# Kernel tuning notes

Hardware: AMD Instinct MI355X
Metric: run time of the kernel (lower is better)

## Reference

```python
import jax, jax.numpy as jnp
import numpy as np

B, S, E = 32, 128, 128
NQ, NS = 100000, 512
QN, SN = 4, 10
S_MAX = 4
NEG = -1e30


def setup_inputs() -> dict:
    key = jax.random.key(0)
    ks = jax.random.split(key, 24)
    def nrm(k, shape, sc):
        return jax.random.normal(k, shape, jnp.float32) * sc
    inp = {}
    inp['question'] = jax.random.randint(ks[0], (B, S), 0, NQ, jnp.int32)
    inp['response'] = jax.random.randint(ks[1], (B, S), 0, 2, jnp.int32)
    inp['mask'] = jax.random.randint(ks[2], (B, S), 0, 2, jnp.int32)
    inp['q_neighbors'] = jax.random.randint(ks[3], (NQ, QN), 0, NS, jnp.int32)
    inp['s_neighbors'] = jax.random.randint(ks[4], (NS, SN), 0, NQ, jnp.int32)
    sidx = jax.random.randint(ks[5], (NQ, S_MAX), 0, NS, jnp.int32)
    inp['qs_table'] = jnp.zeros((NQ, NS), jnp.float32).at[jnp.arange(NQ)[:, None], sidx].set(1.0)
    inp['emb_q'] = nrm(ks[6], (NQ, E), 1.0)
    inp['emb_s'] = nrm(ks[7], (NS, E), 1.0)
    inp['emb_r'] = nrm(ks[8], (2, E), 1.0)
    s_in = 1.0 / np.sqrt(2 * E).astype(np.float32)
    s_e = 1.0 / np.sqrt(E).astype(np.float32)
    inp['W_ih'] = nrm(ks[9], (4 * E, 2 * E), s_in)
    inp['b_ih'] = nrm(ks[10], (4 * E,), s_in)
    inp['b_hh'] = nrm(ks[11], (4 * E,), s_in)
    inp['W_agg'] = nrm(ks[12], (3, E, E), s_e)
    inp['b_agg'] = nrm(ks[13], (3, E), s_e)
    inp['W_last'] = nrm(ks[14], (E, E), s_e)
    inp['b_last'] = nrm(ks[15], (E,), s_e)
    inp['W_query'] = nrm(ks[16], (E, E), s_e)
    inp['b_query'] = nrm(ks[17], (E,), s_e)
    inp['W_key'] = nrm(ks[18], (E, E), s_e)
    inp['b_key'] = nrm(ks[19], (E,), s_e)
    inp['w_W'] = nrm(ks[20], (2 * E,), s_in)
    inp['b_W'] = nrm(ks[21], (), s_in)
    return inp


def _forward(question, response, mask, q_neighbors, s_neighbors, qs_table,
             emb_q, emb_s, emb_r, W_ih, b_ih, b_hh, W_agg, b_agg, W_last, b_last,
             W_query, b_query, W_key, b_key, w_W, b_W):
    Bq, Sq = question.shape
    Ed = emb_q.shape[1]
    AGG = W_agg.shape[0]
    w_q, w_k = w_W[:Ed], w_W[Ed:]
    c_pad = jnp.tanh(b_query) @ w_k  # attention logit piece of an all-zero padded state
    pos = jnp.arange(Sq)

    def step(state_history, xs):
        t, q_t, r_t, m_t, q_next = xs
        # ---- multi-hop neighbor gather (q -> s -> q -> s) ----
        n1 = q_neighbors[q_t]              # [B,QN] skill ids
        n2 = s_neighbors[n1]               # [B,QN,SN] question ids
        n3 = q_neighbors[n2]               # [B,QN,SN,QN] skill ids
        e = [emb_q[q_t], emb_s[n1], emb_q[n2], emb_s[n3]]
        # triangular mean-aggregate (dropout is identity in eval mode)
        for i in range(AGG):
            for j in range(AGG - i):
                e[j] = jnp.tanh((e[j + 1].mean(-2) + e[j]) @ W_agg[j].T + b_agg[j])
        agg = jnp.tanh(e[0] @ W_last.T + b_last)
        emb_qt = jnp.where((m_t == 1)[:, None], agg, emb_q[q_t])
        # ---- LSTMCell with zero initial (h, c): W_hh @ 0 drops out, b_hh remains ----
        x = jnp.concatenate([emb_qt, emb_r[r_t]], -1)
        gates = x @ W_ih.T + b_ih + b_hh
        gi, gf, gg, go = jnp.split(gates, 4, -1)
        h = jax.nn.sigmoid(go) * jnp.tanh(jax.nn.sigmoid(gi) * jnp.tanh(gg))
        # ---- skills related to next question; zero-padded rows contribute exactly 0 ----
        vals, sidx = jax.lax.top_k(qs_table[q_next], S_MAX)
        emb_sk = emb_s[sidx] * (vals > 0.0)[..., None]
        qs_concat = jnp.concatenate([emb_q[q_next][:, None], emb_sk], 1)  # [B,1+S_MAX,E]
        # ---- hard recap: history steps whose question is a 2-hop neighbor of q_next ----
        q_rel = s_neighbors[q_neighbors[q_next]].reshape(Bq, -1)          # [B,QN*SN]
        matches = (question[:, :, None] == q_rel[:, None, :]).any(-1) & (pos[None, :] < t)
        n_sel = matches.sum(-1)
        P = (jnp.max(n_sel) - n_sel).astype(jnp.float32)  # zero-pad count to per-batch max
        # ---- predict: MLP_W(concat(Q,K)) is rank-1 => logit = a[b,q] + c[b,s] ----
        a = jnp.tanh(qs_concat @ W_key.T + b_key) @ w_q + b_W             # [B,Qd]
        c_hist = jnp.tanh(state_history @ W_query.T + b_query) @ w_k      # [B,S]
        c_cur = jnp.tanh(h @ W_query.T + b_query) @ w_k                   # [B]
        lh = jnp.where(matches[:, None, :], a[:, :, None] + c_hist[:, None, :], NEG)
        lc = a + c_cur[:, None]
        lp = a + c_pad
        m = jnp.maximum(jnp.maximum(lh.max(-1), lc), lp)
        Eh = jnp.exp(lh - m[:, :, None])
        Ec = jnp.exp(lc - m)
        Ep = jnp.exp(lp - m)
        g_hist = jnp.einsum('bqe,bse->bqs', qs_concat, state_history)
        g_cur = jnp.einsum('bqe,be->bq', qs_concat, h)
        denom = Eh.sum(-1) + Ec + P[:, None] * Ep  # zero-pad states counted analytically
        num = (Eh * g_hist).sum(-1) + Ec * g_cur   # pads multiply g=0 -> no numerator term
        y = jax.nn.sigmoid(jnp.sum(num / denom, axis=1))
        # original skips the state write at t == 0 (slot 0 stays zero forever)
        state_history = state_history.at[:, t].set(jnp.where(t > 0, h, jnp.zeros_like(h)))
        return state_history, y

    ts = jnp.arange(Sq - 1)
    xs = (ts, question[:, :-1].T, response[:, :-1].T, mask[:, :-1].T, question[:, 1:].T)
    init = jnp.zeros((Bq, Sq, Ed), jnp.float32)
    _, ys = jax.lax.scan(step, init, xs)
    return jnp.zeros((Bq, Sq), jnp.float32).at[:, 0].set(0.5).at[:, 1:].set(ys.T)


def reference(question, response, mask, q_neighbors, s_neighbors, qs_table,
              emb_q, emb_s, emb_r, W_ih, b_ih, b_hh, W_agg, b_agg, W_last, b_last,
              W_query, b_query, W_key, b_key, w_W, b_W):
    return _forward(question, response, mask, q_neighbors, s_neighbors, qs_table,
                    emb_q, emb_s, emb_r, W_ih, b_ih, b_hh, W_agg, b_agg, W_last, b_last,
                    W_query, b_query, W_key, b_key, w_W, b_W)
```

## Files before the change

kernel.cpp:

```cpp
#include <hip/hip_runtime.h>
#include <stdint.h>

#define NB 32
#define SEQ 128
#define EMB 128
#define NSTEP 127
#define NS 512

__device__ __forceinline__ float ftanh(float x){ float e=__expf(2.f*x); return 1.f-2.f/(e+1.f); }
__device__ __forceinline__ float fsig(float x){ return 1.f/(1.f+__expf(-x)); }
__device__ __forceinline__ float4 ld4(const float* p){ return *(const float4*)p; }

#define FMA4(acc, xv, a0, a1, a2, a3) \
  acc.x = fmaf(xv.x, a0.x, fmaf(xv.y, a1.x, fmaf(xv.z, a2.x, fmaf(xv.w, a3.x, acc.x)))); \
  acc.y = fmaf(xv.x, a0.y, fmaf(xv.y, a1.y, fmaf(xv.z, a2.y, fmaf(xv.w, a3.y, acc.y)))); \
  acc.z = fmaf(xv.x, a0.z, fmaf(xv.y, a1.z, fmaf(xv.z, a2.z, fmaf(xv.w, a3.z, acc.z)))); \
  acc.w = fmaf(xv.x, a0.w, fmaf(xv.y, a1.w, fmaf(xv.z, a2.w, fmaf(xv.w, a3.w, acc.w))));

template<int K, int XS>
__device__ __forceinline__ void gemmKS(const float* __restrict__ WT, int NEtot,
                                       const float* Xl, const float* __restrict__ bias,
                                       float* outb, float* partb)
{
  const int tid = threadIdx.x;
  const int et = tid & 31;
  const int kt = (tid >> 5) & 1;
  const int rg = tid >> 6;
  constexpr int KH = K/2;
  constexpr int G  = KH/4;
  const float* wp = WT + (size_t)kt*KH*NEtot + et*4;
  const float* xr = Xl + (size_t)(rg*2)*XS + kt*KH;
  float4 a0 = {0.f,0.f,0.f,0.f};
  float4 a1 = {0.f,0.f,0.f,0.f};
// ... 23 lines not shown
    float4 o1 = ld4(wb + NEtot);
    float4 o2 = ld4(wb + 2*NEtot);
    float4 o3 = ld4(wb + 3*NEtot);
    float4 xb0 = ld4(xr + 4*(g+1));
    float4 xb1 = ld4(xr + XS + 4*(g+1));
    FMA4(a0, xb0, m0, m1, m2, m3);
    FMA4(a1, xb1, m0, m1, m2, m3);
    m0=o0; m1=o1; m2=o2; m3=o3;
  }
  {
    float4 xa0 = ld4(xr + 4*(G-2));
    float4 xa1 = ld4(xr + XS + 4*(G-2));
    FMA4(a0, xa0, w0, w1, w2, w3);
    FMA4(a1, xa1, w0, w1, w2, w3);
    float4 xb0 = ld4(xr + 4*(G-1));
    float4 xb1 = ld4(xr + XS + 4*(G-1));
    FMA4(a0, xb0, m0, m1, m2, m3);
    FMA4(a1, xb1, m0, m1, m2, m3);
  }
  float* dst;
  if (kt == 0) {
    float4 bb = ld4(bias + et*4);
    a0.x+=bb.x; a0.y+=bb.y; a0.z+=bb.z; a0.w+=bb.w;
    a1.x+=bb.x; a1.y+=bb.y; a1.z+=bb.z; a1.w+=bb.w;
    dst = outb;
  } else {
    dst = partb;
  }
  float* ob = dst + (size_t)(rg*2)*132 + et*4;
  *(float4*)(ob)       = a0;
  *(float4*)(ob + 132) = a1;
}

__global__ __launch_bounds__(256) void k_T(
    const float* __restrict__ W_agg, const float* __restrict__ W_last,
    const float* __restrict__ W_query, const float* __restrict__ W_ih,
    const float* __restrict__ b_ih, const float* __restrict__ b_hh,
    const float* __restrict__ b_query, const float* __restrict__ w_W,
    const float* __restrict__ emb_r,
    float* __restrict__ WT012, float* __restrict__ WLT, float* __restrict__ WQT,
    float* __restrict__ WIHT, float* __restrict__ ER2,
    float* __restrict__ BIH, float* __restrict__ CPAD,
    float* __restrict__ G1, int* __restrict__ Pmaxi)
{
  const int gid = blockIdx.x*256 + threadIdx.x;
  const int gsz = gridDim.x*256;
  for (int i = gid; i < 49152; i += gsz) {
    int j = i >> 14, rem = i & 16383, k = rem >> 7, e = rem & 127;
    WT012[i] = W_agg[j*16384 + e*128 + k];
  }
  for (int i = gid; i < 16384; i += gsz) {
    int k = i >> 7, e = i & 127;
    WLT[i] = W_last[e*128 + k];
    WQT[i] = W_query[e*128 + k];
  }
  for (int i = gid; i < 65536; i += gsz) {
    int k = i >> 9, e = i & 511;
    WIHT[i] = W_ih[e*256 + k];
  }
  for (int i = gid; i < 1024; i += gsz) {
    int r = i >> 9, c = i & 511;
    const float* wcol = W_ih + (size_t)c*256 + 128;
    const float* er = emb_r + r*128;
    float acc = 0.f;
    #pragma unroll 4
    for (int k = 0; k < 128; k += 4) {
      acc = fmaf(er[k], wcol[k],
            fmaf(er[k+1], wcol[k+1],
            fmaf(er[k+2], wcol[k+2],
            fmaf(er[k+3], wcol[k+3], acc))));
    }
    ER2[i] = acc;
  }
  for (int i = gid; i < 65536; i += gsz) G1[i] = 0.f;
  if (gid < 512) BIH[gid] = b_ih[gid] + b_hh[gid];
  if (gid < 128) Pmaxi[gid] = 0;
  if (blockIdx.x == 0) {
    __shared__ float red[256];
    float v = (threadIdx.x < 128) ? ftanh(b_query[threadIdx.x]) * w_W[128 + threadIdx.x] : 0.f;
    red[threadIdx.x] = v; __syncthreads();
    #pragma unroll
    for (int s = 128; s > 0; s >>= 1) {
      if (threadIdx.x < s) red[threadIdx.x] += red[threadIdx.x + s];
      __syncthreads();
    }
    if (threadIdx.x == 0) CPAD[0] = red[0];
  }
}

__global__ __launch_bounds__(512) void k_pre(
    const int* __restrict__ s_neighbors, const int* __restrict__ q_neighbors,
    const float* __restrict__ emb_q, const float* __restrict__ emb_s,
    const float* __restrict__ WT012, const float* __restrict__ b_agg,
    float* __restrict__ E1, float* __restrict__ G1)
{
  __shared__ float XA[16*132];
  __shared__ float XB[16*132];
  __shared__ float PB[16*132];
  __shared__ int idx[160];
  __shared__ int n3[64];
  const int tid = threadIdx.x;
  const int blk = blockIdx.x;
  if (blk < 32) {
    const int s0 = blk*16;
    if (tid < 160) idx[tid] = s_neighbors[s0*10 + tid];
    __syncthreads();
    {
      const int e4 = (tid & 31) << 2;
      const int rr = tid >> 5;
      float4 a = ld4(emb_s + (size_t)(s0+rr)*128 + e4);
      float sx=0,sy=0,sz=0,sw=0;
      #pragma unroll
      for (int jj = 0; jj < 10; ++jj) {
        float4 q = ld4(emb_q + (size_t)idx[rr*10+jj]*128 + e4);
        sx+=q.x; sy+=q.y; sz+=q.z; sw+=q.w;
      }
      float4 o; o.x=a.x+0.1f*sx; o.y=a.y+0.1f*sy; o.z=a.z+0.1f*sz; o.w=a.w+0.1f*sw;
      *(float4*)(XA + rr*132 + e4) = o;
    }
    __syncthreads();
    gemmKS<128,132>(WT012 + 16384, 128, XA, b_agg + 128, XB, PB);
    __syncthreads();
    for (int f = tid; f < 2048; f += 512) {
      int r = f >> 7, e = f & 127, i = r*132 + e;
      E1[(size_t)(s0+r)*128 + e] = ftanh(XB[i] + PB[i]);
    }
  } else {
    const int p0 = (blk-32)*16;
    if (tid < 16) idx[tid] = s_neighbors[p0 + tid];
    __syncthreads();
    if (tid < 64) n3[tid] = q_neighbors[(size_t)idx[tid>>2]*4 + (tid&3)];
    __syncthreads();
    {
      const int e4 = (tid & 31) << 2;
      const int rr = tid >> 5;
      float4 a = ld4(emb_q + (size_t)idx[rr]*128 + e4);
      float sx=0,sy=0,sz=0,sw=0;
      #pragma unroll
      for (int k = 0; k < 4; ++k) {
        float4 q = ld4(emb_s + (size_t)n3[rr*4+k]*128 + e4);
        sx+=q.x; sy+=q.y; sz+=q.z; sw+=q.w;
      }
      float4 o; o.x=a.x+0.25f*sx; o.y=a.y+0.25f*sy; o.z=a.z+0.25f*sz; o.w=a.w+0.25f*sw;
      *(float4*)(XA + rr*132 + e4) = o;
    }
    __syncthreads();
    gemmKS<128,132>(WT012 + 32768, 128, XA, b_agg + 256, XB, PB);
    __syncthreads();
    for (int f = tid; f < 2048; f += 512) {
      int r = f >> 7, e = f & 127, i = r*132 + e;
      atomicAdd(&G1[(size_t)((p0+r)/10)*128 + e], ftanh(XB[i] + PB[i]));
    }
  }
}

__global__ __launch_bounds__(512) void k_pre2(
    const float* __restrict__ E1, const float* __restrict__ G1,
    const float* __restrict__ WT012, const float* __restrict__ b_agg,
    float* __restrict__ E2)
{
  __shared__ float XA[16*132];
  __shared__ float XB[16*132];
  __shared__ float PB[16*132];
  const int tid = threadIdx.x;
  const int s0 = blockIdx.x*16;
  for (int f = tid; f < 2048; f += 512) {
    int r = f >> 7, e = f & 127;
    XA[r*132 + e] = 0.1f*G1[(size_t)(s0+r)*128 + e] + E1[(size_t)(s0+r)*128 + e];
  }
  __syncthreads();
  gemmKS<128,132>(WT012 + 16384, 128, XA, b_agg + 128, XB, PB);
  __syncthreads();
  for (int f = tid; f < 2048; f += 512) {
    int r = f >> 7, e = f & 127, i = r*132 + e;
    E2[(size_t)(s0+r)*128 + e] = ftanh(XB[i] + PB[i]);
  }
}

__global__ __launch_bounds__(512) void k_chain(
    const int* __restrict__ question, const int* __restrict__ response,
    const int* __restrict__ maskp, const int* __restrict__ q_neighbors,
    const int* __restrict__ s_neighbors,
    const float* __restrict__ emb_q, const float* __restrict__ emb_s,
    const float* __restrict__ WT012, const float* __restrict__ WLT,
    const float* __restrict__ WQT, const float* __restrict__ WIHT,
    const float* __restrict__ ER2, const float* __restrict__ BIH,
    const float* __restrict__ b_agg, const float* __restrict__ b_last,
    const float* __restrict__ b_query, const float* __restrict__ w_W,
    const float* __restrict__ E1, const float* __restrict__ E2,
    float* __restrict__ Hfull, float* __restrict__ Cq,
    int* __restrict__ nsel, unsigned long long* __restrict__ mwords,
    int* __restrict__ Pmaxi)
{
  __shared__ float XA[16*132];
  __shared__ float XB[16*132];
  __shared__ float M1[16*132];
  __shared__ float M2[16*132];
  __shared__ float PB[16*132];
  __shared__ float XC[16*132];
  __shared__ int qts[16], rts[16], mts[16], n1s[64];

  const int tid = threadIdx.x;
  const int blk = blockIdx.x;

  if (tid < 16) {
    int rid = blk*16 + tid;
    int b = rid / 127, t = rid - b*127;
    qts[tid] = question[b*SEQ + t];
    rts[tid] = response[b*SEQ + t];
    mts[tid] = maskp[b*SEQ + t];
  }
  __syncthreads();
  if (tid < 64) n1s[tid] = q_neighbors[(size_t)qts[tid>>2]*4 + (tid&3)];
  __syncthreads();
  {
    const int e4 = (tid & 31) << 2;
    const int rr = tid >> 5;
    const int* nn = n1s + rr*4;
    float4 a = ld4(emb_q + (size_t)qts[rr]*128 + e4);
    float s1x=0,s1y=0,s1z=0,s1w=0, s2x=0,s2y=0,s2z=0,s2w=0, s3x=0,s3y=0,s3z=0,s3w=0;
    #pragma unroll
    for (int i = 0; i < 4; ++i) {
      float4 q1 = ld4(emb_s + (size_t)nn[i]*128 + e4);
      float4 q2 = ld4(E1 + (size_t)nn[i]*128 + e4);
      float4 q3 = ld4(E2 + (size_t)nn[i]*128 + e4);
      s1x+=q1.x; s1y+=q1.y; s1z+=q1.z; s1w+=q1.w;
      s2x+=q2.x; s2y+=q2.y; s2z+=q2.z; s2w+=q2.w;
      s3x+=q3.x; s3y+=q3.y; s3z+=q3.z; s3w+=q3.w;
    }
    float4 o; o.x=a.x+0.25f*s1x; o.y=a.y+0.25f*s1y; o.z=a.z+0.25f*s1z; o.w=a.w+0.25f*s1w;
    *(float4*)(XA + rr*132 + e4) = o;
    float4 p; p.x=0.25f*s2x; p.y=0.25f*s2y; p.z=0.25f*s2z; p.w=0.25f*s2w;
    *(float4*)(M1 + rr*132 + e4) = p;
    float4 u; u.x=0.25f*s3x; u.y=0.25f*s3y; u.z=0.25f*s3z; u.w=0.25f*s3w;
    *(float4*)(M2 + rr*132 + e4) = u;
  }
  __syncthreads();
  gemmKS<128,132>(WT012, 128, XA, b_agg, XB, PB);
  __syncthreads();
  for (int f = tid; f < 2048; f += 512) {
    int i = (f >> 7)*132 + (f & 127);
    XB[i] = M1[i] + ftanh(XB[i] + PB[i]);
  }
  __syncthreads();
  gemmKS<128,132>(WT012, 128, XB, b_agg, XA, PB);
  __syncthreads();
  for (int f = tid; f < 2048; f += 512) {
    int i = (f >> 7)*132 + (f & 127);
    XA[i] = M2[i] + ftanh(XA[i] + PB[i]);
  }
  __syncthreads();
  gemmKS<128,132>(WT012, 128, XA, b_agg, XB, PB);
  __syncthreads();
  for (int f = tid; f < 2048; f += 512) {
    int i = (f >> 7)*132 + (f & 127);
    XB[i] = ftanh(XB[i] + PB[i]);
  }
  __syncthreads();
  gemmKS<128,132>(WLT, 128, XB, b_last, XA, PB);
  __syncthreads();
  for (int f = tid; f < 2048; f += 512) {
    int r = f >> 7, e = f & 127, i = r*132 + e;
    float agg = ftanh(XA[i] + PB[i]);
    XC[i] = (mts[r] == 1) ? agg : emb_q[(size_t)qts[r]*128 + e];
  }
  __syncthreads();
  gemmKS<128,132>(WIHT,       512, XC, BIH,       XA, PB);
  __syncthreads();
  for (int f = tid; f < 2048; f += 512) {
    int r = f >> 7, e = f & 127, i = r*132 + e;
    XA[i] += PB[i] + ER2[rts[r]*512 + e];
  }
  __syncthreads();
  gemmKS<128,132>(WIHT + 256, 512, XC, BIH + 256, XB, PB);
  __syncthreads();
  for (int f = tid; f < 2048; f += 512) {
    int r = f >> 7, e = f & 127, i = r*132 + e;
    XB[i] += PB[i] + ER2[rts[r]*512 + 256 + e];
  }
  __syncthreads();
  gemmKS<128,132>(WIHT + 384, 512, XC, BIH + 384, M1, PB);
  __syncthreads();
  for (int f = tid; f < 2048; f += 512) {
    int r = f >> 7, e = f & 127, i = r*132 + e;
    float gi = XA[i], gg = XB[i];
    float go = M1[i] + PB[i] + ER2[rts[r]*512 + 384 + e];
    float h = fsig(go) * ftanh(fsig(gi) * ftanh(gg));
    XC[i] = h;
    Hfull[(size_t)(blk*16 + r)*128 + e] = h;
  }
  __syncthreads();
  gemmKS<128,132>(WQT, 128, XC, b_query, XA, PB);
  __syncthreads();
  {
    const int et = tid & 31, rr = tid >> 5;
    float4 wv = ld4(w_W + 128 + et*4);
    float4 o = ld4(XA + rr*132 + et*4);
    float4 p = ld4(PB + rr*132 + et*4);
    float s = ftanh(o.x+p.x)*wv.x + ftanh(o.y+p.y)*wv.y
            + ftanh(o.z+p.z)*wv.z + ftanh(o.w+p.w)*wv.w;
    #pragma unroll
    for (int off = 16; off > 0; off >>= 1) s += __shfl_down(s, off);
    if (et == 0) Cq[blk*16 + rr] = s;
  }
  {
    const int wv = tid >> 6;
    const int ln = tid & 63;
    for (int rr = wv; rr < 16; rr += 8) {
      int rid = blk*16 + rr;
      int b = rid / 127, t = rid - b*127;
      int q_next = question[b*SEQ + t + 1];
      int qrv = 0;
      if (ln < 40)
        qrv = s_neighbors[(size_t)q_neighbors[(size_t)q_next*4 + ln/10]*10 + ln%10];
      int q0 = question[b*SEQ + ln];
      int q1 = question[b*SEQ + 64 + ln];
      bool p0 = false, p1 = false;
      #pragma unroll 8
      for (int i = 0; i < 40; ++i) {
        int qv = __shfl(qrv, i);
        p0 |= (q0 == qv); p1 |= (q1 == qv);
      }
      p0 &= (ln < t);
      p1 &= (64 + ln < t);
      unsigned long long w0 = __ballot(p0);
      unsigned long long w1 = __ballot(p1);
      if (ln == 0) {
        size_t bt = (size_t)b*NSTEP + t;
        mwords[bt*2 + 0] = w0;
        mwords[bt*2 + 1] = w1;
        int ns = __popcll(w0) + __popcll(w1);
        nsel[bt] = ns;
        atomicMax(&Pmaxi[t], ns);
      }
    }
  }
}

__device__ __forceinline__ float wredsum(float v) {
  #pragma unroll
  for (int o = 32; o > 0; o >>= 1) v += __shfl_down(v, o);
  return v;
}
__device__ __forceinline__ float wredmax(float v) {
  #pragma unroll
  for (int o = 32; o > 0; o >>= 1) v = fmaxf(v, __shfl_down(v, o));
  return v;
}

__global__ __launch_bounds__(128) void k_attn(
    const int* __restrict__ question, const float* __restrict__ qs_table,
    const float* __restrict__ emb_q, const float* __restrict__ emb_s,
    const float* __restrict__ CPAD,
    const float* __restrict__ Hfull, const float* __restrict__ Cq,
    const int* __restrict__ nsel, const unsigned long long* __restrict__ mwords,
    const int* __restrict__ Pmaxi, float* __restrict__ out)
{
  __shared__ float us[128];
  __shared__ int cols[8];
  __shared__ int cnt;
  __shared__ float smx[2];
  __shared__ float s3[2][3];
  const int tid = threadIdx.x;
  const int wid = tid >> 6;
  const int bid = blockIdx.x;
  const int b = bid / NSTEP, t = bid % NSTEP;
  const size_t bt = (size_t)b*NSTEP + t;
  const int q_next = question[b*SEQ + t + 1];

  if (tid == 0) cnt = 0;
  __syncthreads();
  {
    float4 v = ld4(qs_table + (size_t)q_next*NS + tid*4);
    if (v.x > 0.f) { int p = atomicAdd(&cnt, 1); if (p < 8) cols[p] = tid*4; }
    if (v.y > 0.f) { int p = atomicAdd(&cnt, 1); if (p < 8) cols[p] = tid*4+1; }
    if (v.z > 0.f) { int p = atomicAdd(&cnt, 1); if (p < 8) cols[p] = tid*4+2; }
    if (v.w > 0.f) { int p = atomicAdd(&cnt, 1); if (p < 8) cols[p] = tid*4+3; }
  }
  __syncthreads();
  const int nc = min(cnt, 4);
  {
    float ue = emb_q[(size_t)q_next*EMB + tid];
    for (int i = 0; i < nc; ++i) ue += emb_s[(size_t)cols[i]*EMB + tid];
    us[tid] = ue;
  }
  const float c_pad = CPAD[0];
  const float P = (float)(Pmaxi[t] - nsel[bt]);

  const unsigned long long w0 = mwords[bt*2 + 0];
  const unsigned long long w1 = mwords[bt*2 + 1];
  const bool matched = (tid < 64) ? ((w0 >> tid) & 1ull)
                                  : ((w1 >> (tid - 64)) & 1ull);
  const float c_cur = Cq[bt];
  float Cp = matched ? ((tid == 0) ? c_pad : Cq[(size_t)b*NSTEP + tid]) : -3.0e38f;
  float mh = wredmax(Cp);
  if ((tid & 63) == 0) smx[wid] = mh;
  __syncthreads();
  float M = fmaxf(fmaxf(smx[0], smx[1]), fmaxf(c_cur, c_pad));
  float wgt = matched ? __expf(Cp - M) : 0.f;
  float dotp = 0.f;
  if (matched && tid >= 1) {
    const float* hp = Hfull + ((size_t)b*NSTEP + tid)*EMB;
    float s = 0.f;
    #pragma unroll 8
    for (int e = 0; e < 128; e += 4) {
      float4 h4 = ld4(hp + e);
      s = fmaf(us[e],h4.x, fmaf(us[e+1],h4.y, fmaf(us[e+2],h4.z, fmaf(us[e+3],h4.w, s))));
    }
    dotp = s;
  }
  float gcp = us[tid] * Hfull[bt*EMB + tid];
  float a0 = wredsum(wgt);
  float a1 = wredsum(wgt * dotp);
  float a2 = wredsum(gcp);
  if ((tid & 63) == 0) { s3[wid][0] = a0; s3[wid][1] = a1; s3[wid][2] = a2; }
  __syncthreads();
  if (tid == 0) {
    float Sexp = s3[0][0] + s3[1][0];
    float Snum = s3[0][1] + s3[1][1];
    float gc   = s3[0][2] + s3[1][2];
    float Ec = __expf(c_cur - M), Ep = __expf(c_pad - M);
    float D = Sexp + Ec + P * Ep;
    float numt = Snum + Ec * gc;
    out[b*SEQ + t + 1] = fsig(numt / D);
    if (t == 0) out[b*SEQ] = 0.5f;
  }
}

extern "C" void kernel_launch(void* const* d_in, const int* in_sizes, int n_in,
                              void* d_out, int out_size, void* d_ws, size_t ws_size,
                              hipStream_t stream) {
  const int* question    = (const int*)d_in[0];
  const int* response    = (const int*)d_in[1];
  const int* maskp       = (const int*)d_in[2];
  const int* q_neighbors = (const int*)d_in[3];
  const int* s_neighbors = (const int*)d_in[4];
  const float* qs_table  = (const float*)d_in[5];
  const float* emb_q     = (const float*)d_in[6];
  const float* emb_s     = (const float*)d_in[7];
  const float* emb_r     = (const float*)d_in[8];
  const float* W_ih      = (const float*)d_in[9];
  const float* b_ih      = (const float*)d_in[10];
  const float* b_hh      = (const float*)d_in[11];
  const float* W_agg     = (const float*)d_in[12];
  const float* b_agg     = (const float*)d_in[13];
  const float* W_last    = (const float*)d_in[14];
  const float* b_last    = (const float*)d_in[15];
  const float* W_query   = (const float*)d_in[16];
  const float* b_query   = (const float*)d_in[17];
  const float* w_W       = (const float*)d_in[20];
  float* out = (float*)d_out;

  float* ws = (float*)d_ws;
  float* WT012 = ws;
  float* WLT   = ws + 49152;
  float* WQT   = ws + 65536;
  float* WIHT  = ws + 81920;
  float* ER2   = ws + 147456;
  float* BIH   = ws + 212992;
  float* CPAD  = ws + 213504;
  float* E1    = ws + 213520;
  float* G1    = ws + 279056;
  float* E2    = ws + 344592;
  float* Hfull = ws + 410128;
  float* Cq    = ws + 930320;
  int*   Pmaxi = (int*)(ws + 934384);
  int*   nselp = (int*)(ws + 934512);
  unsigned long long* mwords =
      (unsigned long long*)(((uintptr_t)(ws + 938576) + 15) & ~(uintptr_t)15);

  k_T<<<dim3(512), dim3(256), 0, stream>>>(
      W_agg, W_last, W_query, W_ih, b_ih, b_hh, b_query, w_W, emb_r,
      WT012, WLT, WQT, WIHT, ER2, BIH, CPAD, G1, Pmaxi);
  k_pre<<<dim3(352), dim3(512), 0, stream>>>(
      s_neighbors, q_neighbors, emb_q, emb_s, WT012, b_agg, E1, G1);
  k_pre2<<<dim3(32), dim3(512), 0, stream>>>(E1, G1, WT012, b_agg, E2);
  k_chain<<<dim3(254), dim3(512), 0, stream>>>(
      question, response, maskp, q_neighbors, s_neighbors, emb_q, emb_s,
      WT012, WLT, WQT, WIHT, ER2, BIH, b_agg, b_last, b_query, w_W,
      E1, E2, Hfull, Cq, nselp, mwords, Pmaxi);
  k_attn<<<dim3(NB*NSTEP), dim3(128), 0, stream>>>(
      question, qs_table, emb_q, emb_s, CPAD, Hfull, Cq,
      nselp, mwords, Pmaxi, out);
}
```

Measured before the change: 382.3 us.

## Fuse four pre-attention kernels into one cooperative kernel with grid syncs

```diff
diff --git a/kernel.cpp b/kernel.cpp
--- a/kernel.cpp
+++ b/kernel.cpp
@@ -1,4 +1,5 @@
 #include <hip/hip_runtime.h>
+#include <hip/hip_cooperative_groups.h>
 #include <stdint.h>
 
 #define NB 32
@@ -88,36 +89,61 @@
   *(float4*)(ob + 132) = a1;
 }
 
-__global__ __launch_bounds__(256) void k_T(
-    const float* __restrict__ W_agg, const float* __restrict__ W_last,
-    const float* __restrict__ W_query, const float* __restrict__ W_ih,
-    const float* __restrict__ b_ih, const float* __restrict__ b_hh,
-    const float* __restrict__ b_query, const float* __restrict__ w_W,
-    const float* __restrict__ emb_r,
-    float* __restrict__ WT012, float* __restrict__ WLT, float* __restrict__ WQT,
-    float* __restrict__ WIHT, float* __restrict__ ER2,
-    float* __restrict__ BIH, float* __restrict__ CPAD,
-    float* __restrict__ G1, int* __restrict__ Pmaxi)
+struct KParams {
+  const int *question, *response, *maskp, *q_neighbors, *s_neighbors;
+  const float *emb_q, *emb_s, *emb_r;
+  const float *W_agg, *W_last, *W_query, *W_ih, *b_ih, *b_hh, *b_agg,
+              *b_last, *b_query, *w_W;
+  float *WT012, *WLT, *WQT, *WIHT, *ER2, *BIH, *CPAD, *E1, *G1, *E2,
+        *Hfull, *Cq;
+  int *nsel;
+  unsigned long long *mwords;
+  int *Pmaxi;
+};
+
+__global__ __launch_bounds__(512) void k_fused(KParams p)
 {
-  const int gid = blockIdx.x*256 + threadIdx.x;
-  const int gsz = gridDim.x*256;
+  namespace cg = cooperative_groups;
+  cg::grid_group grid = cg::this_grid();
+
+  __shared__ float smf[16*132*6];
+  __shared__ int   smi[352];
+
+  const int tid = threadIdx.x;
+  const int blk = blockIdx.x;
+  const int gid = blk*512 + tid;
+  const int gsz = 256*512;
+
+  float* XA = smf;
+  float* XB = smf + 2112;
+  float* M1 = smf + 4224;
+  float* M2 = smf + 6336;
+  float* PB = smf + 8448;
+  float* XC = smf + 10560;
+  int* idx = smi;
+  int* n3  = smi + 160;
+  int* qts = smi + 224;
+  int* rts = smi + 240;
+  int* mts = smi + 256;
+  int* n1s = smi + 272;
+
   for (int i = gid; i < 49152; i += gsz) {
     int j = i >> 14, rem = i & 16383, k = rem >> 7, e = rem & 127;
-    WT012[i] = W_agg[j*16384 + e*128 + k];
+    p.WT012[i] = p.W_agg[j*16384 + e*128 + k];
   }
   for (int i = gid; i < 16384; i += gsz) {
     int k = i >> 7, e = i & 127;
-    WLT[i] = W_last[e*128 + k];
-    WQT[i] = W_query[e*128 + k];
+    p.WLT[i] = p.W_last[e*128 + k];
+    p.WQT[i] = p.W_query[e*128 + k];
   }
   for (int i = gid; i < 65536; i += gsz) {
     int k = i >> 9, e = i & 511;
-    WIHT[i] = W_ih[e*256 + k];
+    p.WIHT[i] = p.W_ih[e*256 + k];
   }
   for (int i = gid; i < 1024; i += gsz) {
     int r = i >> 9, c = i & 511;
-    const float* wcol = W_ih + (size_t)c*256 + 128;
-    const float* er = emb_r + r*128;
+    const float* wcol = p.W_ih + (size_t)c*256 + 128;
+    const float* er = p.emb_r + r*128;
     float acc = 0.f;
     #pragma unroll 4
     for (int k = 0; k < 128; k += 4) {
@@ -126,268 +152,228 @@
             fmaf(er[k+2], wcol[k+2],
             fmaf(er[k+3], wcol[k+3], acc))));
     }
-    ER2[i] = acc;
-  }
-  for (int i = gid; i < 65536; i += gsz) G1[i] = 0.f;
-  if (gid < 512) BIH[gid] = b_ih[gid] + b_hh[gid];
-  if (gid < 128) Pmaxi[gid] = 0;
-  if (blockIdx.x == 0) {
-    __shared__ float red[256];
-    float v = (threadIdx.x < 128) ? ftanh(b_query[threadIdx.x]) * w_W[128 + threadIdx.x] : 0.f;
-    red[threadIdx.x] = v; __syncthreads();
+    p.ER2[i] = acc;
+  }
+  for (int i = gid; i < 65536; i += gsz) p.G1[i] = 0.f;
+  if (gid < 512) p.BIH[gid] = p.b_ih[gid] + p.b_hh[gid];
+  if (gid < 128) p.Pmaxi[gid] = 0;
+  if (blk == 0) {
+    float v = (tid < 128) ? ftanh(p.b_query[tid]) * p.w_W[128 + tid] : 0.f;
+    if (tid < 256) smf[tid] = v;
+    __syncthreads();
     #pragma unroll
     for (int s = 128; s > 0; s >>= 1) {
-      if (threadIdx.x < s) red[threadIdx.x] += red[threadIdx.x + s];
-      __syncthreads();
-    }
-    if (threadIdx.x == 0) CPAD[0] = red[0];
-  }
-}
-
-__global__ __launch_bounds__(512) void k_pre(
-    const int* __restrict__ s_neighbors, const int* __restrict__ q_neighbors,
-    const float* __restrict__ emb_q, const float* __restrict__ emb_s,
-    const float* __restrict__ WT012, const float* __restrict__ b_agg,
-    float* __restrict__ E1, float* __restrict__ G1)
-{
-  __shared__ float XA[16*132];
-  __shared__ float XB[16*132];
-  __shared__ float PB[16*132];
-  __shared__ int idx[160];
-  __shared__ int n3[64];
-  const int tid = threadIdx.x;
-  const int blk = blockIdx.x;
+      if (tid < s) smf[tid] += smf[tid + s];
+      __syncthreads();
+    }
+    if (tid == 0) p.CPAD[0] = smf[0];
+  }
+  grid.sync();
+
+  for (int vb = blk; vb < 352; vb += 256) {
+    if (vb < 32) {
+      const int s0 = vb*16;
+      if (tid < 160) idx[tid] = p.s_neighbors[s0*10 + tid];
+      __syncthreads();
+      {
+        const int e4 = (tid & 31) << 2;
+        const int rr = tid >> 5;
+        float4 a = ld4(p.emb_s + (size_t)(s0+rr)*128 + e4);
+        float sx=0,sy=0,sz=0,sw=0;
+        #pragma unroll
+        for (int jj = 0; jj < 10; ++jj) {
+          float4 q = ld4(p.emb_q + (size_t)idx[rr*10+jj]*128 + e4);
+          sx+=q.x; sy+=q.y; sz+=q.z; sw+=q.w;
+        }
+        float4 o; o.x=a.x+0.1f*sx; o.y=a.y+0.1f*sy; o.z=a.z+0.1f*sz; o.w=a.w+0.1f*sw;
+        *(float4*)(XA + rr*132 + e4) = o;
+      }
+      __syncthreads();
+      gemmKS<128,132>(p.WT012 + 16384, 128, XA, p.b_agg + 128, XB, PB);
+      __syncthreads();
+      for (int f = tid; f < 2048; f += 512) {
+        int r = f >> 7, e = f & 127, i = r*132 + e;
+        p.E1[(size_t)(s0+r)*128 + e] = ftanh(XB[i] + PB[i]);
+      }
+      __syncthreads();
+    } else {
+      const int p0 = (vb-32)*16;
+      if (tid < 16) idx[tid] = p.s_neighbors[p0 + tid];
+      __syncthreads();
+      if (tid < 64) n3[tid] = p.q_neighbors[(size_t)idx[tid>>2]*4 + (tid&3)];
+      __syncthreads();
+      {
+        const int e4 = (tid & 31) << 2;
+        const int rr = tid >> 5;
+        float4 a = ld4(p.emb_q + (size_t)idx[rr]*128 + e4);
+        float sx=0,sy=0,sz=0,sw=0;
+        #pragma unroll
+        for (int k = 0; k < 4; ++k) {
+          float4 q = ld4(p.emb_s + (size_t)n3[rr*4+k]*128 + e4);
+          sx+=q.x; sy+=q.y; sz+=q.z; sw+=q.w;
+        }
+        float4 o; o.x=a.x+0.25f*sx; o.y=a.y+0.25f*sy; o.z=a.z+0.25f*sz; o.w=a.w+0.25f*sw;
+        *(float4*)(XA + rr*132 + e4) = o;
+      }
+      __syncthreads();
+      gemmKS<128,132>(p.WT012 + 32768, 128, XA, p.b_agg + 256, XB, PB);
+      __syncthreads();
+      for (int f = tid; f < 2048; f += 512) {
+        int r = f >> 7, e = f & 127, i = r*132 + e;
+        atomicAdd(&p.G1[(size_t)((p0+r)/10)*128 + e], ftanh(XB[i] + PB[i]));
+      }
+      __syncthreads();
+    }
+  }
+  grid.sync();
+
   if (blk < 32) {
     const int s0 = blk*16;
-    if (tid < 160) idx[tid] = s_neighbors[s0*10 + tid];
+    for (int f = tid; f < 2048; f += 512) {
+      int r = f >> 7, e = f & 127;
+      XA[r*132 + e] = 0.1f*p.G1[(size_t)(s0+r)*128 + e] + p.E1[(size_t)(s0+r)*128 + e];
+    }
+    __syncthreads();
+    gemmKS<128,132>(p.WT012 + 16384, 128, XA, p.b_agg + 128, XB, PB);
+    __syncthreads();
+    for (int f = tid; f < 2048; f += 512) {
+      int r = f >> 7, e = f & 127, i = r*132 + e;
+      p.E2[(size_t)(s0+r)*128 + e] = ftanh(XB[i] + PB[i]);
+    }
+  }
+  grid.sync();
+
+  if (blk < 254) {
+    if (tid < 16) {
+      int rid = blk*16 + tid;
+      int b = rid / 127, t = rid - b*127;
+      qts[tid] = p.question[b*SEQ + t];
+      rts[tid] = p.response[b*SEQ + t];
+      mts[tid] = p.maskp[b*SEQ + t];
+    }
+    __syncthreads();
+    if (tid < 64) n1s[tid] = p.q_neighbors[(size_t)qts[tid>>2]*4 + (tid&3)];
     __syncthreads();
     {
       const int e4 = (tid & 31) << 2;
       const int rr = tid >> 5;
-      float4 a = ld4(emb_s + (size_t)(s0+rr)*128 + e4);
-      float sx=0,sy=0,sz=0,sw=0;
+      const int* nn = n1s + rr*4;
+      float4 a = ld4(p.emb_q + (size_t)qts[rr]*128 + e4);
+      float s1x=0,s1y=0,s1z=0,s1w=0, s2x=0,s2y=0,s2z=0,s2w=0, s3x=0,s3y=0,s3z=0,s3w=0;
       #pragma unroll
-      for (int jj = 0; jj < 10; ++jj) {
-        float4 q = ld4(emb_q + (size_t)idx[rr*10+jj]*128 + e4);
-        sx+=q.x; sy+=q.y; sz+=q.z; sw+=q.w;
+      for (int i = 0; i < 4; ++i) {
+        float4 q1 = ld4(p.emb_s + (size_t)nn[i]*128 + e4);
+        float4 q2 = ld4(p.E1 + (size_t)nn[i]*128 + e4);
+        float4 q3 = ld4(p.E2 + (size_t)nn[i]*128 + e4);
+        s1x+=q1.x; s1y+=q1.y; s1z+=q1.z; s1w+=q1.w;
+        s2x+=q2.x; s2y+=q2.y; s2z+=q2.z; s2w+=q2.w;
+        s3x+=q3.x; s3y+=q3.y; s3z+=q3.z; s3w+=q3.w;
       }
-      float4 o; o.x=a.x+0.1f*sx; o.y=a.y+0.1f*sy; o.z=a.z+0.1f*sz; o.w=a.w+0.1f*sw;
+      float4 o; o.x=a.x+0.25f*s1x; o.y=a.y+0.25f*s1y; o.z=a.z+0.25f*s1z; o.w=a.w+0.25f*s1w;
       *(float4*)(XA + rr*132 + e4) = o;
-    }
-    __syncthreads();
-    gemmKS<128,132>(WT012 + 16384, 128, XA, b_agg + 128, XB, PB);
+      float4 pv; pv.x=0.25f*s2x; pv.y=0.25f*s2y; pv.z=0.25f*s2z; pv.w=0.25f*s2w;
+      *(float4*)(M1 + rr*132 + e4) = pv;
+      float4 u; u.x=0.25f*s3x; u.y=0.25f*s3y; u.z=0.25f*s3z; u.w=0.25f*s3w;
+      *(float4*)(M2 + rr*132 + e4) = u;
+    }
+    __syncthreads();
+    gemmKS<128,132>(p.WT012, 128, XA, p.b_agg, XB, PB);
+    __syncthreads();
+    for (int f = tid; f < 2048; f += 512) {
+      int i = (f >> 7)*132 + (f & 127);
+      XB[i] = M1[i] + ftanh(XB[i] + PB[i]);
+    }
+    __syncthreads();
+    gemmKS<128,132>(p.WT012, 128, XB, p.b_agg, XA, PB);
+    __syncthreads();
+    for (int f = tid; f < 2048; f += 512) {
+      int i = (f >> 7)*132 + (f & 127);
+      XA[i] = M2[i] + ftanh(XA[i] + PB[i]);
+    }
+    __syncthreads();
+    gemmKS<128,132>(p.WT012, 128, XA, p.b_agg, XB, PB);
+    __syncthreads();
+    for (int f = tid; f < 2048; f += 512) {
+      int i = (f >> 7)*132 + (f & 127);
+      XB[i] = ftanh(XB[i] + PB[i]);
+    }
+    __syncthreads();
+    gemmKS<128,132>(p.WLT, 128, XB, p.b_last, XA, PB);
     __syncthreads();
     for (int f = tid; f < 2048; f += 512) {
       int r = f >> 7, e = f & 127, i = r*132 + e;
-      E1[(size_t)(s0+r)*128 + e] = ftanh(XB[i] + PB[i]);
-    }
-  } else {
-    const int p0 = (blk-32)*16;
-    if (tid < 16) idx[tid] = s_neighbors[p0 + tid];
-    __syncthreads();
-    if (tid < 64) n3[tid] = q_neighbors[(size_t)idx[tid>>2]*4 + (tid&3)];
+      float agg = ftanh(XA[i] + PB[i]);
+      XC[i] = (mts[r] == 1) ? agg : p.emb_q[(size_t)qts[r]*128 + e];
+    }
+    __syncthreads();
+    gemmKS<128,132>(p.WIHT,       512, XC, p.BIH,       XA, PB);
+    __syncthreads();
+    for (int f = tid; f < 2048; f += 512) {
+      int r = f >> 7, e = f & 127, i = r*132 + e;
+      XA[i] += PB[i] + p.ER2[rts[r]*512 + e];
+    }
+    __syncthreads();
+    gemmKS<128,132>(p.WIHT + 256, 512, XC, p.BIH + 256, XB, PB);
+    __syncthreads();
+    for (int f = tid; f < 2048; f += 512) {
+      int r = f >> 7, e = f & 127, i = r*132 + e;
+      XB[i] += PB[i] + p.ER2[rts[r]*512 + 256 + e];
+    }
+    __syncthreads();
+    gemmKS<128,132>(p.WIHT + 384, 512, XC, p.BIH + 384, M1, PB);
+    __syncthreads();
+    for (int f = tid; f < 2048; f += 512) {
+      int r = f >> 7, e = f & 127, i = r*132 + e;
+      float gi = XA[i], gg = XB[i];
+      float go = M1[i] + PB[i] + p.ER2[rts[r]*512 + 384 + e];
+      float h = fsig(go) * ftanh(fsig(gi) * ftanh(gg));
+      XC[i] = h;
+      p.Hfull[(size_t)(blk*16 + r)*128 + e] = h;
+    }
+    __syncthreads();
+    gemmKS<128,132>(p.WQT, 128, XC, p.b_query, XA, PB);
     __syncthreads();
     {
-      const int e4 = (tid & 31) << 2;
-      const int rr = tid >> 5;
-      float4 a = ld4(emb_q + (size_t)idx[rr]*128 + e4);
-      float sx=0,sy=0,sz=0,sw=0;
+      const int et = tid & 31, rr = tid >> 5;
+      float4 wv = ld4(p.w_W + 128 + et*4);
+      float4 o = ld4(XA + rr*132 + et*4);
+      float4 pv = ld4(PB + rr*132 + et*4);
+      float s = ftanh(o.x+pv.x)*wv.x + ftanh(o.y+pv.y)*wv.y
+              + ftanh(o.z+pv.z)*wv.z + ftanh(o.w+pv.w)*wv.w;
       #pragma unroll
-      for (int k = 0; k < 4; ++k) {
-        float4 q = ld4(emb_s + (size_t)n3[rr*4+k]*128 + e4);
-        sx+=q.x; sy+=q.y; sz+=q.z; sw+=q.w;
-      }
-      float4 o; o.x=a.x+0.25f*sx; o.y=a.y+0.25f*sy; o.z=a.z+0.25f*sz; o.w=a.w+0.25f*sw;
-      *(float4*)(XA + rr*132 + e4) = o;
-    }
-    __syncthreads();
-    gemmKS<128,132>(WT012 + 32768, 128, XA, b_agg + 256, XB, PB);
-    __syncthreads();
-    for (int f = tid; f < 2048; f += 512) {
-      int r = f >> 7, e = f & 127, i = r*132 + e;
-      atomicAdd(&G1[(size_t)((p0+r)/10)*128 + e], ftanh(XB[i] + PB[i]));
-    }
-  }
-}
-
-__global__ __launch_bounds__(512) void k_pre2(
-    const float* __restrict__ E1, const float* __restrict__ G1,
-    const float* __restrict__ WT012, const float* __restrict__ b_agg,
-    float* __restrict__ E2)
-{
-  __shared__ float XA[16*132];
-  __shared__ float XB[16*132];
-  __shared__ float PB[16*132];
-  const int tid = threadIdx.x;
-  const int s0 = blockIdx.x*16;
-  for (int f = tid; f < 2048; f += 512) {
-    int r = f >> 7, e = f & 127;
-    XA[r*132 + e] = 0.1f*G1[(size_t)(s0+r)*128 + e] + E1[(size_t)(s0+r)*128 + e];
-  }
-  __syncthreads();
-  gemmKS<128,132>(WT012 + 16384, 128, XA, b_agg + 128, XB, PB);
-  __syncthreads();
-  for (int f = tid; f < 2048; f += 512) {
-    int r = f >> 7, e = f & 127, i = r*132 + e;
-    E2[(size_t)(s0+r)*128 + e] = ftanh(XB[i] + PB[i]);
-  }
-}
-
-__global__ __launch_bounds__(512) void k_chain(
-    const int* __restrict__ question, const int* __restrict__ response,
-    const int* __restrict__ maskp, const int* __restrict__ q_neighbors,
-    const int* __restrict__ s_neighbors,
-    const float* __restrict__ emb_q, const float* __restrict__ emb_s,
-    const float* __restrict__ WT012, const float* __restrict__ WLT,
-    const float* __restrict__ WQT, const float* __restrict__ WIHT,
-    const float* __restrict__ ER2, const float* __restrict__ BIH,
-    const float* __restrict__ b_agg, const float* __restrict__ b_last,
-    const float* __restrict__ b_query, const float* __restrict__ w_W,
-    const float* __restrict__ E1, const float* __restrict__ E2,
-    float* __restrict__ Hfull, float* __restrict__ Cq,
-    int* __restrict__ nsel, unsigned long long* __restrict__ mwords,
-    int* __restrict__ Pmaxi)
-{
-  __shared__ float XA[16*132];
-  __shared__ float XB[16*132];
-  __shared__ float M1[16*132];
-  __shared__ float M2[16*132];
-  __shared__ float PB[16*132];
-  __shared__ float XC[16*132];
-  __shared__ int qts[16], rts[16], mts[16], n1s[64];
-
-  const int tid = threadIdx.x;
-  const int blk = blockIdx.x;
-
-  if (tid < 16) {
-    int rid = blk*16 + tid;
-    int b = rid / 127, t = rid - b*127;
-    qts[tid] = question[b*SEQ + t];
-    rts[tid] = response[b*SEQ + t];
-    mts[tid] = maskp[b*SEQ + t];
-  }
-  __syncthreads();
-  if (tid < 64) n1s[tid] = q_neighbors[(size_t)qts[tid>>2]*4 + (tid&3)];
-  __syncthreads();
-  {
-    const int e4 = (tid & 31) << 2;
-    const int rr = tid >> 5;
-    const int* nn = n1s + rr*4;
-    float4 a = ld4(emb_q + (size_t)qts[rr]*128 + e4);
-    float s1x=0,s1y=0,s1z=0,s1w=0, s2x=0,s2y=0,s2z=0,s2w=0, s3x=0,s3y=0,s3z=0,s3w=0;
-    #pragma unroll
-    for (int i = 0; i < 4; ++i) {
-      float4 q1 = ld4(emb_s + (size_t)nn[i]*128 + e4);
-      float4 q2 = ld4(E1 + (size_t)nn[i]*128 + e4);
-      float4 q3 = ld4(E2 + (size_t)nn[i]*128 + e4);
-      s1x+=q1.x; s1y+=q1.y; s1z+=q1.z; s1w+=q1.w;
-      s2x+=q2.x; s2y+=q2.y; s2z+=q2.z; s2w+=q2.w;
-      s3x+=q3.x; s3y+=q3.y; s3z+=q3.z; s3w+=q3.w;
-    }
-    float4 o; o.x=a.x+0.25f*s1x; o.y=a.y+0.25f*s1y; o.z=a.z+0.25f*s1z; o.w=a.w+0.25f*s1w;
-    *(float4*)(XA + rr*132 + e4) = o;
-    float4 p; p.x=0.25f*s2x; p.y=0.25f*s2y; p.z=0.25f*s2z; p.w=0.25f*s2w;
-    *(float4*)(M1 + rr*132 + e4) = p;
-    float4 u; u.x=0.25f*s3x; u.y=0.25f*s3y; u.z=0.25f*s3z; u.w=0.25f*s3w;
-    *(float4*)(M2 + rr*132 + e4) = u;
-  }
-  __syncthreads();
-  gemmKS<128,132>(WT012, 128, XA, b_agg, XB, PB);
-  __syncthreads();
-  for (int f = tid; f < 2048; f += 512) {
-    int i = (f >> 7)*132 + (f & 127);
-    XB[i] = M1[i] + ftanh(XB[i] + PB[i]);
-  }
-  __syncthreads();
-  gemmKS<128,132>(WT012, 128, XB, b_agg, XA, PB);
-  __syncthreads();
-  for (int f = tid; f < 2048; f += 512) {
-    int i = (f >> 7)*132 + (f & 127);
-    XA[i] = M2[i] + ftanh(XA[i] + PB[i]);
-  }
-  __syncthreads();
-  gemmKS<128,132>(WT012, 128, XA, b_agg, XB, PB);
-  __syncthreads();
-  for (int f = tid; f < 2048; f += 512) {
-    int i = (f >> 7)*132 + (f & 127);
-    XB[i] = ftanh(XB[i] + PB[i]);
-  }
-  __syncthreads();
-  gemmKS<128,132>(WLT, 128, XB, b_last, XA, PB);
-  __syncthreads();
-  for (int f = tid; f < 2048; f += 512) {
-    int r = f >> 7, e = f & 127, i = r*132 + e;
-    float agg = ftanh(XA[i] + PB[i]);
-    XC[i] = (mts[r] == 1) ? agg : emb_q[(size_t)qts[r]*128 + e];
-  }
-  __syncthreads();
-  gemmKS<128,132>(WIHT,       512, XC, BIH,       XA, PB);
-  __syncthreads();
-  for (int f = tid; f < 2048; f += 512) {
-    int r = f >> 7, e = f & 127, i = r*132 + e;
-    XA[i] += PB[i] + ER2[rts[r]*512 + e];
-  }
-  __syncthreads();
-  gemmKS<128,132>(WIHT + 256, 512, XC, BIH + 256, XB, PB);
-  __syncthreads();
-  for (int f = tid; f < 2048; f += 512) {
-    int r = f >> 7, e = f & 127, i = r*132 + e;
-    XB[i] += PB[i] + ER2[rts[r]*512 + 256 + e];
-  }
-  __syncthreads();
-  gemmKS<128,132>(WIHT + 384, 512, XC, BIH + 384, M1, PB);
-  __syncthreads();
-  for (int f = tid; f < 2048; f += 512) {
-    int r = f >> 7, e = f & 127, i = r*132 + e;
-    float gi = XA[i], gg = XB[i];
-    float go = M1[i] + PB[i] + ER2[rts[r]*512 + 384 + e];
-    float h = fsig(go) * ftanh(fsig(gi) * ftanh(gg));
-    XC[i] = h;
-    Hfull[(size_t)(blk*16 + r)*128 + e] = h;
-  }
-  __syncthreads();
-  gemmKS<128,132>(WQT, 128, XC, b_query, XA, PB);
-  __syncthreads();
-  {
-    const int et = tid & 31, rr = tid >> 5;
-    float4 wv = ld4(w_W + 128 + et*4);
-    float4 o = ld4(XA + rr*132 + et*4);
-    float4 p = ld4(PB + rr*132 + et*4);
-    float s = ftanh(o.x+p.x)*wv.x + ftanh(o.y+p.y)*wv.y
-            + ftanh(o.z+p.z)*wv.z + ftanh(o.w+p.w)*wv.w;
-    #pragma unroll
-    for (int off = 16; off > 0; off >>= 1) s += __shfl_down(s, off);
-    if (et == 0) Cq[blk*16 + rr] = s;
-  }
-  {
-    const int wv = tid >> 6;
-    const int ln = tid & 63;
-    for (int rr = wv; rr < 16; rr += 8) {
-      int rid = blk*16 + rr;
-      int b = rid / 127, t = rid - b*127;
-      int q_next = question[b*SEQ + t + 1];
-      int qrv = 0;
-      if (ln < 40)
-        qrv = s_neighbors[(size_t)q_neighbors[(size_t)q_next*4 + ln/10]*10 + ln%10];
-      int q0 = question[b*SEQ + ln];
-      int q1 = question[b*SEQ + 64 + ln];
-      bool p0 = false, p1 = false;
-      #pragma unroll 8
-      for (int i = 0; i < 40; ++i) {
-        int qv = __shfl(qrv, i);
-        p0 |= (q0 == qv); p1 |= (q1 == qv);
-      }
-      p0 &= (ln < t);
-      p1 &= (64 + ln < t);
-      unsigned long long w0 = __ballot(p0);
-      unsigned long long w1 = __ballot(p1);
-      if (ln == 0) {
-        size_t bt = (size_t)b*NSTEP + t;
-        mwords[bt*2 + 0] = w0;
-        mwords[bt*2 + 1] = w1;
-        int ns = __popcll(w0) + __popcll(w1);
-        nsel[bt] = ns;
-        atomicMax(&Pmaxi[t], ns);
+      for (int off = 16; off > 0; off >>= 1) s += __shfl_down(s, off);
+      if (et == 0) p.Cq[blk*16 + rr] = s;
+    }
+    {
+      const int wv = tid >> 6;
+      const int ln = tid & 63;
+      for (int rr = wv; rr < 16; rr += 8) {
+        int rid = blk*16 + rr;
+        int b = rid / 127, t = rid - b*127;
+        int q_next = p.question[b*SEQ + t + 1];
+        int qrv = 0;
+        if (ln < 40)
+          qrv = p.s_neighbors[(size_t)p.q_neighbors[(size_t)q_next*4 + ln/10]*10 + ln%10];
+        int q0 = p.question[b*SEQ + ln];
+        int q1 = p.question[b*SEQ + 64 + ln];
+        bool p0 = false, p1 = false;
+        #pragma unroll 8
+        for (int i = 0; i < 40; ++i) {
+          int qv = __shfl(qrv, i);
+          p0 |= (q0 == qv); p1 |= (q1 == qv);
+        }
+        p0 &= (ln < t);
+        p1 &= (64 + ln < t);
+        unsigned long long w0 = __ballot(p0);
+        unsigned long long w1 = __ballot(p1);
+        if (ln == 0) {
+          size_t bt = (size_t)b*NSTEP + t;
+          p.mwords[bt*2 + 0] = w0;
+          p.mwords[bt*2 + 1] = w1;
+          int ns = __popcll(w0) + __popcll(w1);
+          p.nsel[bt] = ns;
+          atomicMax(&p.Pmaxi[t], ns);
+        }
       }
     }
   }
@@ -428,10 +414,10 @@
   __syncthreads();
   {
     float4 v = ld4(qs_table + (size_t)q_next*NS + tid*4);
-    if (v.x > 0.f) { int p = atomicAdd(&cnt, 1); if (p < 8) cols[p] = tid*4; }
-    if (v.y > 0.f) { int p = atomicAdd(&cnt, 1); if (p < 8) cols[p] = tid*4+1; }
-    if (v.z > 0.f) { int p = atomicAdd(&cnt, 1); if (p < 8) cols[p] = tid*4+2; }
-    if (v.w > 0.f) { int p = atomicAdd(&cnt, 1); if (p < 8) cols[p] = tid*4+3; }
+    if (v.x > 0.f) { int pp = atomicAdd(&cnt, 1); if (pp < 8) cols[pp] = tid*4; }
+    if (v.y > 0.f) { int pp = atomicAdd(&cnt, 1); if (pp < 8) cols[pp] = tid*4+1; }
+    if (v.z > 0.f) { int pp = atomicAdd(&cnt, 1); if (pp < 8) cols[pp] = tid*4+2; }
+    if (v.w > 0.f) { int pp = atomicAdd(&cnt, 1); if (pp < 8) cols[pp] = tid*4+3; }
   }
   __syncthreads();
   const int nc = min(cnt, 4);
@@ -525,16 +511,21 @@
   unsigned long long* mwords =
       (unsigned long long*)(((uintptr_t)(ws + 938576) + 15) & ~(uintptr_t)15);
 
-  k_T<<<dim3(512), dim3(256), 0, stream>>>(
-      W_agg, W_last, W_query, W_ih, b_ih, b_hh, b_query, w_W, emb_r,
-      WT012, WLT, WQT, WIHT, ER2, BIH, CPAD, G1, Pmaxi);
-  k_pre<<<dim3(352), dim3(512), 0, stream>>>(
-      s_neighbors, q_neighbors, emb_q, emb_s, WT012, b_agg, E1, G1);
-  k_pre2<<<dim3(32), dim3(512), 0, stream>>>(E1, G1, WT012, b_agg, E2);
-  k_chain<<<dim3(254), dim3(512), 0, stream>>>(
-      question, response, maskp, q_neighbors, s_neighbors, emb_q, emb_s,
-      WT012, WLT, WQT, WIHT, ER2, BIH, b_agg, b_last, b_query, w_W,
-      E1, E2, Hfull, Cq, nselp, mwords, Pmaxi);
+  KParams p;
+  p.question = question; p.response = response; p.maskp = maskp;
+  p.q_neighbors = q_neighbors; p.s_neighbors = s_neighbors;
+  p.emb_q = emb_q; p.emb_s = emb_s; p.emb_r = emb_r;
+  p.W_agg = W_agg; p.W_last = W_last; p.W_query = W_query; p.W_ih = W_ih;
+  p.b_ih = b_ih; p.b_hh = b_hh; p.b_agg = b_agg; p.b_last = b_last;
+  p.b_query = b_query; p.w_W = w_W;
+  p.WT012 = WT012; p.WLT = WLT; p.WQT = WQT; p.WIHT = WIHT; p.ER2 = ER2;
+  p.BIH = BIH; p.CPAD = CPAD; p.E1 = E1; p.G1 = G1; p.E2 = E2;
+  p.Hfull = Hfull; p.Cq = Cq; p.nsel = nselp; p.mwords = mwords;
+  p.Pmaxi = Pmaxi;
+
+  void* kargs[] = { (void*)&p };
+  hipLaunchCooperativeKernel((const void*)k_fused, dim3(256), dim3(512),
+                             kargs, 0, stream);
   k_attn<<<dim3(NB*NSTEP), dim3(128), 0, stream>>>(
       question, qs_table, emb_q, emb_s, CPAD, Hfull, Cq,
       nselp, mwords, Pmaxi, out);
```

Result: slower. 502.1 us (+31.3%).

## Remap attention kernel to one wavefront per (batch, step) with ballot-based column scan

Applied to the files above, without the earlier changes.

```diff
diff --git a/kernel.cpp b/kernel.cpp
--- a/kernel.cpp
+++ b/kernel.cpp
@@ -393,18 +393,18 @@
   }
 }
 
-__device__ __forceinline__ float wredsum(float v) {
+__device__ __forceinline__ float xsum(float v) {
   #pragma unroll
-  for (int o = 32; o > 0; o >>= 1) v += __shfl_down(v, o);
+  for (int o = 32; o > 0; o >>= 1) v += __shfl_xor(v, o);
   return v;
 }
-__device__ __forceinline__ float wredmax(float v) {
+__device__ __forceinline__ float xmax(float v) {
   #pragma unroll
-  for (int o = 32; o > 0; o >>= 1) v = fmaxf(v, __shfl_down(v, o));
+  for (int o = 32; o > 0; o >>= 1) v = fmaxf(v, __shfl_xor(v, o));
   return v;
 }
 
-__global__ __launch_bounds__(128) void k_attn(
+__global__ __launch_bounds__(512) void k_attn(
     const int* __restrict__ question, const float* __restrict__ qs_table,
     const float* __restrict__ emb_q, const float* __restrict__ emb_s,
     const float* __restrict__ CPAD,
@@ -412,69 +412,96 @@
     const int* __restrict__ nsel, const unsigned long long* __restrict__ mwords,
     const int* __restrict__ Pmaxi, float* __restrict__ out)
 {
-  __shared__ float us[128];
-  __shared__ int cols[8];
-  __shared__ int cnt;
-  __shared__ float smx[2];
-  __shared__ float s3[2][3];
+  __shared__ float us[8][128];
   const int tid = threadIdx.x;
-  const int wid = tid >> 6;
-  const int bid = blockIdx.x;
-  const int b = bid / NSTEP, t = bid % NSTEP;
+  const int wv = tid >> 6;
+  const int ln = tid & 63;
+  const int pid = blockIdx.x*8 + wv;
+  const int b = pid / NSTEP, t = pid - b*NSTEP;
   const size_t bt = (size_t)b*NSTEP + t;
   const int q_next = question[b*SEQ + t + 1];
 
-  if (tid == 0) cnt = 0;
-  __syncthreads();
+  float4 v0 = ld4(qs_table + (size_t)q_next*NS + ln*4);
+  float4 v1 = ld4(qs_table + (size_t)q_next*NS + 256 + ln*4);
+  unsigned long long m0b = __ballot(v0.x > 0.f);
+  unsigned long long m1b = __ballot(v0.y > 0.f);
+  unsigned long long m2b = __ballot(v0.z > 0.f);
+  unsigned long long m3b = __ballot(v0.w > 0.f);
+  unsigned long long m4b = __ballot(v1.x > 0.f);
+  unsigned long long m5b = __ballot(v1.y > 0.f);
+  unsigned long long m6b = __ballot(v1.z > 0.f);
+  unsigned long long m7b = __ballot(v1.w > 0.f);
+
+  float ue0 = emb_q[(size_t)q_next*EMB + ln];
+  float ue1 = emb_q[(size_t)q_next*EMB + 64 + ln];
   {
-    float4 v = ld4(qs_table + (size_t)q_next*NS + tid*4);
-    if (v.x > 0.f) { int p = atomicAdd(&cnt, 1); if (p < 8) cols[p] = tid*4; }
-    if (v.y > 0.f) { int p = atomicAdd(&cnt, 1); if (p < 8) cols[p] = tid*4+1; }
-    if (v.z > 0.f) { int p = atomicAdd(&cnt, 1); if (p < 8) cols[p] = tid*4+2; }
-    if (v.w > 0.f) { int p = atomicAdd(&cnt, 1); if (p < 8) cols[p] = tid*4+3; }
-  }
-  __syncthreads();
-  const int nc = min(cnt, 4);
-  {
-    float ue = emb_q[(size_t)q_next*EMB + tid];
-    for (int i = 0; i < nc; ++i) ue += emb_s[(size_t)cols[i]*EMB + tid];
-    us[tid] = ue;
-  }
+    int added = 0;
+    unsigned long long mm[1];
+    #define SCAN(MB, KOFF, BASE) \
+      { unsigned long long m = MB; \
+        while (m && added < 4) { \
+          int i = __ffsll((unsigned long long)m) - 1; m &= m - 1ull; \
+          int c = BASE + i*4 + KOFF; \
+          ue0 += emb_s[(size_t)c*EMB + ln]; \
+          ue1 += emb_s[(size_t)c*EMB + 64 + ln]; \
+          ++added; } }
+    SCAN(m0b, 0, 0) SCAN(m1b, 1, 0) SCAN(m2b, 2, 0) SCAN(m3b, 3, 0)
+    SCAN(m4b, 0, 256) SCAN(m5b, 1, 256) SCAN(m6b, 2, 256) SCAN(m7b, 3, 256)
+    #undef SCAN
+    (void)mm;
+  }
+  us[wv][ln] = ue0;
+  us[wv][64 + ln] = ue1;
+
   const float c_pad = CPAD[0];
   const float P = (float)(Pmaxi[t] - nsel[bt]);
-
+  const float c_cur = Cq[bt];
   const unsigned long long w0 = mwords[bt*2 + 0];
   const unsigned long long w1 = mwords[bt*2 + 1];
-  const bool matched = (tid < 64) ? ((w0 >> tid) & 1ull)
-                                  : ((w1 >> (tid - 64)) & 1ull);
-  const float c_cur = Cq[bt];
-  float Cp = matched ? ((tid == 0) ? c_pad : Cq[(size_t)b*NSTEP + tid]) : -3.0e38f;
-  float mh = wredmax(Cp);
-  if ((tid & 63) == 0) smx[wid] = mh;
-  __syncthreads();
-  float M = fmaxf(fmaxf(smx[0], smx[1]), fmaxf(c_cur, c_pad));
-  float wgt = matched ? __expf(Cp - M) : 0.f;
-  float dotp = 0.f;
-  if (matched && tid >= 1) {
-    const float* hp = Hfull + ((size_t)b*NSTEP + tid)*EMB;
-    float s = 0.f;
-    #pragma unroll 8
-    for (int e = 0; e < 128; e += 4) {
-      float4 h4 = ld4(hp + e);
-      s = fmaf(us[e],h4.x, fmaf(us[e+1],h4.y, fmaf(us[e+2],h4.z, fmaf(us[e+3],h4.w, s))));
-    }
-    dotp = s;
-  }
-  float gcp = us[tid] * Hfull[bt*EMB + tid];
-  float a0 = wredsum(wgt);
-  float a1 = wredsum(wgt * dotp);
-  float a2 = wredsum(gcp);
-  if ((tid & 63) == 0) { s3[wid][0] = a0; s3[wid][1] = a1; s3[wid][2] = a2; }
-  __syncthreads();
-  if (tid == 0) {
-    float Sexp = s3[0][0] + s3[1][0];
-    float Snum = s3[0][1] + s3[1][1];
-    float gc   = s3[0][2] + s3[1][2];
+
+  float gcp = ue0*Hfull[bt*EMB + ln] + ue1*Hfull[bt*EMB + 64 + ln];
+  float gc = xsum(gcp);
+
+  float M, Sexp = 0.f, Snum = 0.f;
+  if ((w0 | w1) == 0ull) {
+    M = fmaxf(c_cur, c_pad);
+  } else {
+    const bool ma = (w0 >> ln) & 1ull;
+    const bool mb = (w1 >> ln) & 1ull;
+    float Cp0 = ma ? ((ln == 0) ? c_pad : Cq[(size_t)b*NSTEP + ln]) : -3.0e38f;
+    float Cp1 = mb ? Cq[(size_t)b*NSTEP + 64 + ln] : -3.0e38f;
+    float mh = xmax(fmaxf(Cp0, Cp1));
+    M = fmaxf(mh, fmaxf(c_cur, c_pad));
+    float wgt0 = ma ? __expf(Cp0 - M) : 0.f;
+    float wgt1 = mb ? __expf(Cp1 - M) : 0.f;
+    __threadfence_block();
+    float d0 = 0.f, d1 = 0.f;
+    if (ma && ln >= 1) {
+      const float* hp = Hfull + ((size_t)b*NSTEP + ln)*EMB;
+      const float* uu = us[wv];
+      float s = 0.f;
+      #pragma unroll 8
+      for (int e = 0; e < 128; e += 4) {
+        float4 h4 = ld4(hp + e);
+        s = fmaf(uu[e],h4.x, fmaf(uu[e+1],h4.y, fmaf(uu[e+2],h4.z, fmaf(uu[e+3],h4.w, s))));
+      }
+      d0 = s;
+    }
+    if (mb) {
+      const float* hp = Hfull + ((size_t)b*NSTEP + 64 + ln)*EMB;
+      const float* uu = us[wv];
+      float s = 0.f;
+      #pragma unroll 8
+      for (int e = 0; e < 128; e += 4) {
+        float4 h4 = ld4(hp + e);
+        s = fmaf(uu[e],h4.x, fmaf(uu[e+1],h4.y, fmaf(uu[e+2],h4.z, fmaf(uu[e+3],h4.w, s))));
+      }
+      d1 = s;
+    }
+    Sexp = xsum(wgt0 + wgt1);
+    Snum = xsum(fmaf(wgt0, d0, wgt1 * d1));
+  }
+  if (ln == 0) {
     float Ec = __expf(c_cur - M), Ep = __expf(c_pad - M);
     float D = Sexp + Ec + P * Ep;
     float numt = Snum + Ec * gc;
@@ -535,7 +562,7 @@
       question, response, maskp, q_neighbors, s_neighbors, emb_q, emb_s,
       WT012, WLT, WQT, WIHT, ER2, BIH, b_agg, b_last, b_query, w_W,
       E1, E2, Hfull, Cq, nselp, mwords, Pmaxi);
-  k_attn<<<dim3(NB*NSTEP), dim3(128), 0, stream>>>(
+  k_attn<<<dim3(508), dim3(512), 0, stream>>>(
       question, qs_table, emb_q, emb_s, CPAD, Hfull, Cq,
       nselp, mwords, Pmaxi, out);
 }
```

Result: no change. 381.2 us (-0.3%).
